# Optimization experiments

Hardware: AMD Instinct MI355X
Metric: run time of the kernel (lower is better)

Reference implementation:

```python
import jax, jax.numpy as jnp
import numpy as np

SEQ_LEN = 4096
EMBED_DIM = 1280
NUM_HEADS = 16
HEAD_DIM = EMBED_DIM // NUM_HEADS  # 80
SCALING = float(np.sqrt(HEAD_DIM))  # NOTE: source multiplies by sqrt(head_dim)
NEG_INF = float(np.finfo(np.float32).min)


def rotate_half(x):
    x1, x2 = jnp.split(x, 2, axis=-1)
    return jnp.concatenate((-x2, x1), axis=-1)


def setup_inputs() -> dict:
    key = jax.random.key(0)
    ks = jax.random.split(key, 7)
    s = 0.02
    hidden_states = jax.random.normal(ks[0], (SEQ_LEN, EMBED_DIM), dtype=jnp.float32)
    w_qkv = jax.random.normal(ks[1], (3 * EMBED_DIM, EMBED_DIM), dtype=jnp.float32) * s
    b_qkv = jax.random.normal(ks[2], (3 * EMBED_DIM,), dtype=jnp.float32) * s
    w_proj = jax.random.normal(ks[3], (EMBED_DIM, EMBED_DIM), dtype=jnp.float32) * s
    b_proj = jax.random.normal(ks[4], (EMBED_DIM,), dtype=jnp.float32) * s
    # rotary angles: theta duplicated to head_dim (emb = cat(rope, rope))
    inv_freq = 1.0 / (10000.0 ** (jnp.arange(0, HEAD_DIM // 2, dtype=jnp.float32) * 2.0 / HEAD_DIM))
    pos = jnp.arange(SEQ_LEN, dtype=jnp.float32)
    freqs = pos[:, None] * inv_freq[None, :]            # [S, hd/2]
    emb = jnp.concatenate((freqs, freqs), axis=-1)       # [S, hd]
    cos = jnp.cos(emb)
    sin = jnp.sin(emb)
    # 4 packed images of 1024 patches each
    cu_seqlens = jnp.array([0, 1024, 2048, 3072, 4096], dtype=jnp.int32)
    return {
        "hidden_states": hidden_states,
        "w_qkv": w_qkv, "b_qkv": b_qkv,
        "w_proj": w_proj, "b_proj": b_proj,
        "cos": cos, "sin": sin,
        "cu_seqlens": cu_seqlens,
    }


def reference(hidden_states, w_qkv, b_qkv, w_proj, b_proj, cos, sin, cu_seqlens):
    S = hidden_states.shape[0]
    # packed QKV projection
    qkv = hidden_states @ w_qkv.T + b_qkv                  # [S, 3D]
    qkv = qkv.reshape(S, 3, NUM_HEADS, HEAD_DIM)
    q, k, v = qkv[:, 0], qkv[:, 1], qkv[:, 2]              # [S, H, hd]
    # fp32 RoPE (broadcast cos/sin over heads)
    c = cos[:, None, :].astype(jnp.float32)
    sn = sin[:, None, :].astype(jnp.float32)
    qf, kf = q.astype(jnp.float32), k.astype(jnp.float32)
    q = (qf * c + rotate_half(qf) * sn).astype(q.dtype)
    k = (kf * c + rotate_half(kf) * sn).astype(k.dtype)
    # block-diagonal mask from cu_seqlens: same segment -> 0, else -inf
    pos = jnp.arange(S)
    seg = jnp.searchsorted(cu_seqlens, pos, side="right") - 1  # [S]
    bias = jnp.where(seg[:, None] == seg[None, :], 0.0, NEG_INF)  # [S, S]
    # dense attention over whole packed sequence (as in source)
    scores = jnp.einsum("shd,thd->hst", q, k) * SCALING + bias[None]
    weights = jax.nn.softmax(scores.astype(jnp.float32), axis=-1).astype(q.dtype)
    attn = jnp.einsum("hst,thd->shd", weights, v).reshape(S, EMBED_DIM)
    return attn @ w_proj.T + b_proj
```

## Files before the change

kernel.cpp:

```cpp
#include <hip/hip_runtime.h>

#define SEQ   4096
#define EMB   1280
#define NH    16
#define HD    80
#define HDP   96
#define O3    3840
#define SEGLEN 1024
#define NSEG  4
#define QSCALE (8.94427190999915878564f * 1.44269504088896340736f)

typedef unsigned short u16;
typedef __attribute__((ext_vector_type(8))) _Float16 f16x8;
typedef __attribute__((ext_vector_type(4))) _Float16 f16x4;
typedef __attribute__((ext_vector_type(2))) __fp16   h16x2;
typedef __attribute__((ext_vector_type(4))) float    f32x4;

__device__ __forceinline__ float ex2(float x) { return __builtin_amdgcn_exp2f(x); }

__device__ __forceinline__ u16 f2h(float f) {
  union { _Float16 h; u16 u; } v; v.h = (_Float16)f; return v.u;
}
__device__ __forceinline__ float h2f(u16 b) {
  union { u16 u; _Float16 h; } v; v.u = b; return (float)v.h;
}
__device__ __forceinline__ f32x4 exp2_4(f32x4 x) {
  f32x4 r; r.x = ex2(x.x); r.y = ex2(x.y); r.z = ex2(x.z); r.w = ex2(x.w); return r;
}
__device__ __forceinline__ f16x4 pk4(f32x4 s) {
  union { h16x2 h[2]; f16x4 f; } u;
  u.h[0] = __builtin_amdgcn_cvt_pkrtz(s.x, s.y);
  u.h[1] = __builtin_amdgcn_cvt_pkrtz(s.z, s.w);
  return u.f;
}
__device__ __forceinline__ void gl2lds16(const u16* g, u16* l) {
  __builtin_amdgcn_global_load_lds(
      (const __attribute__((address_space(1))) unsigned int*)g,
      (__attribute__((address_space(3))) unsigned int*)l, 16, 0, 0);
}

#define CVT_N1 (SEQ * EMB / 4)
#define CVT_N2 (O3 * EMB / 4)
#define CVT_N3 (EMB * EMB / 4)
__global__ void cvt_all_kernel(const float* __restrict__ a, const float* __restrict__ b,
                               const float* __restrict__ c, u16* __restrict__ oa,
                               u16* __restrict__ ob, u16* __restrict__ oc) {
  int i = blockIdx.x * blockDim.x + threadIdx.x;
  const float* src; u16* dst; int j = i;
  if (j < CVT_N1)                { src = a; dst = oa; }
  else if (j < CVT_N1 + CVT_N2)  { src = b; dst = ob; j -= CVT_N1; }
  else                           { src = c; dst = oc; j -= CVT_N1 + CVT_N2; }
  float4 f = ((const float4*)src)[j];
  union { u16 h[4]; uint2 v; } o;
  o.h[0] = f2h(f.x); o.h[1] = f2h(f.y); o.h[2] = f2h(f.z); o.h[3] = f2h(f.w);
  ((uint2*)dst)[j] = o.v;
}

template<int OUTF>
__global__ __launch_bounds__(256)
void gemm_bias_kernel(const u16* __restrict__ A, const u16* __restrict__ W,
                      const float* __restrict__ bias, void* __restrict__ Cout,
                      int N, int K) {
  __shared__ u16 As[128][64];
  __shared__ u16 Bs[128][64];
  const int tid  = threadIdx.x;
  const int bm   = blockIdx.y, bn = blockIdx.x;
  const int lane = tid & 63;
  const int wid  = tid >> 6;
  const int wm   = (wid >> 1) * 64, wn = (wid & 1) * 64;
  const int lr   = lane & 15, quad = lane >> 4;

  f32x4 acc[4][4];
  const f32x4 z4 = {0.f, 0.f, 0.f, 0.f};
  #pragma unroll
  for (int i = 0; i < 4; ++i)
    #pragma unroll
    for (int j = 0; j < 4; ++j) acc[i][j] = z4;

  const int arow = tid >> 3;
  const int acol = (((tid & 7) ^ (arow & 7)) * 8);
  const u16* Ab = A + (size_t)(bm * 128) * K;
  const u16* Wb = W + (size_t)(bn * 128) * K;
  u16* AsL = &As[0][0] + tid * 8;
  u16* BsL = &Bs[0][0] + tid * 8;

  for (int kt = 0; kt < K; kt += 64) {
    #pragma unroll
    for (int r = 0; r < 4; ++r) {
      gl2lds16(&Ab[(size_t)(arow + r * 32) * K + kt + acol], AsL + r * 2048);
      gl2lds16(&Wb[(size_t)(arow + r * 32) * K + kt + acol], BsL + r * 2048);
    }
    __syncthreads();
    #pragma unroll
    for (int k32 = 0; k32 < 2; ++k32) {
      const int c = (((k32 * 4 + quad) ^ (lr & 7)) * 8);
      f16x8 aF[4], bF[4];
      #pragma unroll
      for (int i = 0; i < 4; ++i) {
        aF[i] = *(const f16x8*)&As[wm + i * 16 + lr][c];
        bF[i] = *(const f16x8*)&Bs[wn + i * 16 + lr][c];
      }
      #pragma unroll
      for (int i = 0; i < 4; ++i)
        #pragma unroll
        for (int j = 0; j < 4; ++j)
          acc[i][j] = __builtin_amdgcn_mfma_f32_16x16x32_f16(aF[i], bF[j], acc[i][j], 0, 0, 0);
    }
    __syncthreads();
  }

  #pragma unroll
  for (int i = 0; i < 4; ++i) {
    int rowb = bm * 128 + wm + i * 16 + quad * 4;
    #pragma unroll
    for (int j = 0; j < 4; ++j) {
      int col = bn * 128 + wn + j * 16 + lr;
      float bv = bias[col];
      #pragma unroll
      for (int r = 0; r < 4; ++r) {
        float v = acc[i][j][r] + bv;
        if (OUTF) ((float*)Cout)[(size_t)(rowb + r) * N + col] = v;
        else      ((u16*)Cout)[(size_t)(rowb + r) * N + col] = f2h(v);
      }
    }
  }
}

__global__ __launch_bounds__(512, 2)
void gemm256_kernel(const u16* __restrict__ A, const u16* __restrict__ W,
                    const float* __restrict__ bias, u16* __restrict__ Cout,
                    int N, int K) {
  __shared__ u16 As[2][256][64];
  __shared__ u16 Bs[2][256][64];
  const int tid  = threadIdx.x;
  const int bm   = blockIdx.y, bn = blockIdx.x;
  const int lane = tid & 63;
  const int wid  = tid >> 6;
  const int wm   = wid >> 2;
  const int wn   = wid & 3;
  const int lr   = lane & 15, quad = lane >> 4;
  const int NT   = K >> 6;

  const u16* Ab = A + (size_t)(bm * 256) * K;
  const u16* Wb = W + (size_t)(bn * 256) * K;

  const int srr  = tid >> 3;
  const int scol = ((tid & 7) ^ (srr & 7)) << 3;
  const u16* ApL = Ab + (size_t)srr * K + scol;
  const u16* WpL = Wb + (size_t)srr * K + scol;

  auto stA = [&](int b, int row0, int t) {
    gl2lds16(ApL + (size_t)row0 * K + t * 64,        &As[b][row0][0]      + tid * 8);
    gl2lds16(ApL + (size_t)(row0 + 64) * K + t * 64, &As[b][row0 + 64][0] + tid * 8);
  };
  auto stB = [&](int b, int row0, int t) {
    gl2lds16(WpL + (size_t)row0 * K + t * 64,        &Bs[b][row0][0]      + tid * 8);
    gl2lds16(WpL + (size_t)(row0 + 64) * K + t * 64, &Bs[b][row0 + 64][0] + tid * 8);
  };

  f32x4 acc[8][4];
  const f32x4 z4 = {0.f, 0.f, 0.f, 0.f};
  #pragma unroll
  for (int i = 0; i < 8; ++i)
    #pragma unroll
    for (int j = 0; j < 4; ++j) acc[i][j] = z4;

  stA(0, 0, 0); stA(0, 128, 0);
  stB(0, 0, 0); stB(0, 128, 0);
  stA(1, 0, 1);
  asm volatile("s_waitcnt vmcnt(2)" ::: "memory");
  __builtin_amdgcn_s_barrier();

  for (int t = 0; t < NT; ++t) {
    const int buf = t & 1, nb = buf ^ 1;
    #pragma unroll
    for (int mq = 0; mq < 2; ++mq) {
      #pragma unroll
      for (int k32 = 0; k32 < 2; ++k32) {
        const int c = (((k32 * 4 + quad) ^ (lr & 7)) << 3);
        f16x8 aF[4], bF[4];
        #pragma unroll
        for (int i = 0; i < 4; ++i)
          aF[i] = *(const f16x8*)&As[buf][mq * 128 + wm * 64 + i * 16 + lr][c];
        #pragma unroll
        for (int j = 0; j < 4; ++j)
          bF[j] = *(const f16x8*)&Bs[buf][wn * 64 + j * 16 + lr][c];
        __builtin_amdgcn_sched_barrier(0);
        if (mq == 0 && k32 == 0) {
          if (t + 1 < NT) { stB(nb, 0, t + 1); stA(nb, 128, t + 1); }
        } else if (mq == 0 && k32 == 1) {
          if (t + 1 < NT) stB(nb, 128, t + 1);
        } else if (mq == 1 && k32 == 0) {
          if (t + 2 < NT) stA(buf, 0, t + 2);
        }
        __builtin_amdgcn_s_barrier();
        asm volatile("s_waitcnt lgkmcnt(0)" ::: "memory");
        __builtin_amdgcn_sched_barrier(0);
        __builtin_amdgcn_s_setprio(1);
        #pragma unroll
        for (int i = 0; i < 4; ++i)
          #pragma unroll
          for (int j = 0; j < 4; ++j)
            acc[mq * 4 + i][j] =
                __builtin_amdgcn_mfma_f32_16x16x32_f16(aF[i], bF[j], acc[mq * 4 + i][j], 0, 0, 0);
        __builtin_amdgcn_s_setprio(0);
        if (mq == 1 && k32 == 1) {
          if (t < NT - 2) asm volatile("s_waitcnt vmcnt(2)" ::: "memory");
          else            asm volatile("s_waitcnt vmcnt(0)" ::: "memory");
        }
        __builtin_amdgcn_s_barrier();
        __builtin_amdgcn_sched_barrier(0);
      }
    }
  }

  #pragma unroll
  for (int mq = 0; mq < 2; ++mq) {
    #pragma unroll
    for (int i = 0; i < 4; ++i) {
      const int rowb = bm * 256 + mq * 128 + wm * 64 + i * 16 + quad * 4;
      #pragma unroll
      for (int j = 0; j < 4; ++j) {
        const int col = bn * 256 + wn * 64 + j * 16 + lr;
        const float bv = bias[col];
        #pragma unroll
        for (int r = 0; r < 4; ++r)
          Cout[(size_t)(rowb + r) * N + col] = f2h(acc[mq * 4 + i][j][r] + bv);
      }
    }
  }
}

__global__ __launch_bounds__(256)
void rope_reorg_kernel(const u16* __restrict__ qkv, const float* __restrict__ cosp,
                       const float* __restrict__ sinp, u16* __restrict__ Qp,
                       u16* __restrict__ Kp, u16* __restrict__ Vt) {
  __shared__ u16 Qs[64][80];
  __shared__ u16 Ks[64][80];
  __shared__ u16 Vs[64][88];
  const int tid = threadIdx.x;
  const int s0 = blockIdx.x * 64;
  const int h  = blockIdx.y;

  for (int t = tid; t < 640; t += 256) {
    int r = t / 10, c = (t % 10) * 8;
    size_t g = (size_t)(s0 + r) * O3 + h * HD + c;
    *(uint4*)&Qs[r][c] = *(const uint4*)&qkv[g];
    *(uint4*)&Ks[r][c] = *(const uint4*)&qkv[g + EMB];
    *(uint4*)&Vs[r][c] = *(const uint4*)&qkv[g + 2 * EMB];
  }
  __syncthreads();

  for (int t = tid; t < 64 * 24; t += 256) {
    int r = t / 24, d4 = (t % 24) * 4;
    int s = s0 + r;
    size_t po = ((size_t)h * SEQ + s) * HDP + d4;
    if (d4 >= HD) {
      uint2 z = make_uint2(0, 0);
      *(uint2*)&Qp[po] = z; *(uint2*)&Kp[po] = z;
      continue;
    }
    float4 cv = *(const float4*)&cosp[(size_t)s * HD + d4];
    float4 sv = *(const float4*)&sinp[(size_t)s * HD + d4];
    int dp4 = (d4 < 40) ? d4 + 40 : d4 - 40;
    float sgn = (d4 < 40) ? -1.f : 1.f;
    union { u16 h[4]; uint2 v; } oq, ok;
    const float* cp = (const float*)&cv;
    const float* sp = (const float*)&sv;
    #pragma unroll
    for (int j = 0; j < 4; ++j) {
      float q  = h2f(Qs[r][d4 + j]),  k  = h2f(Ks[r][d4 + j]);
      float qp = h2f(Qs[r][dp4 + j]), kp = h2f(Ks[r][dp4 + j]);
      oq.h[j] = f2h((q * cp[j] + sgn * qp * sp[j]) * QSCALE);
      ok.h[j] = f2h(k * cp[j] + sgn * kp * sp[j]);
    }
    *(uint2*)&Qp[po] = oq.v;
    *(uint2*)&Kp[po] = ok.v;
  }

  for (int t = tid; t < HD * 8; t += 256) {
    int d = t / 8, sc = (t % 8) * 8;
    union { u16 h[8]; uint4 v; } o;
    #pragma unroll
    for (int j = 0; j < 8; ++j) o.h[j] = Vs[sc + j][d];
    *(uint4*)&Vt[((size_t)(h * HD + d)) * SEQ + s0 + sc] = o.v;
  }
}

__global__ __launch_bounds__(256)
void attn_kernel(const u16* __restrict__ Qp, const u16* __restrict__ Kp,
                 const u16* __restrict__ Vt, u16* __restrict__ attnO) {
  __shared__ u16 K_l[64][96];
  __shared__ u16 V_l[80][64];

  const int tid = threadIdx.x;
  const int lane = tid & 63, w = tid >> 6;
  const int lr = lane & 15, quad = lane >> 4;
  const int h = blockIdx.y, sg = blockIdx.z;
  const int seg0 = sg * SEGLEN;
  const int q0b = seg0 + blockIdx.x * 64;

  f16x8 qF[3];
  {
    int qrow = q0b + w * 16 + lr;
    #pragma unroll
    for (int kc = 0; kc < 3; ++kc)
      qF[kc] = *(const f16x8*)&Qp[((size_t)h * SEQ + qrow) * HDP + kc * 32 + quad * 8];
  }

  const u16* Kbase = Kp + ((size_t)h * SEQ + seg0) * HDP;
  const u16* Vbase = Vt + (size_t)h * HD * SEQ + seg0;
  const u16* pK[3]; u16* dK[3];
  const u16* pV[3]; u16* dV[3];
  #pragma unroll
  for (int t = 0; t < 3; ++t) {
    int s = t * 256 + tid;
    int r = s / 12, c = s % 12;
    pK[t] = Kbase + (size_t)r * HDP + c * 8;
    dK[t] = &K_l[0][0] + s * 8;
    int rv = s / 8, cv = s % 8;
    int cg = cv ^ (rv & 7);
    pV[t] = Vbase + (size_t)rv * SEQ + cg * 8;
    dV[t] = &V_l[0][0] + s * 8;
  }

  const f32x4 z4 = {0.f, 0.f, 0.f, 0.f};
  float m_r = -3.0e38f;
  float l_r = 0.0f;
  f32x4 Oacc[5];
  #pragma unroll
  for (int n = 0; n < 5; ++n) Oacc[n] = z4;

  for (int kt = 0; kt < SEGLEN; kt += 64) {
    gl2lds16(pK[0], dK[0]); gl2lds16(pK[1], dK[1]); gl2lds16(pK[2], dK[2]);
    gl2lds16(pV[0], dV[0]); gl2lds16(pV[1], dV[1]);
    if (tid < 128) gl2lds16(pV[2], dV[2]);
    #pragma unroll
    for (int t = 0; t < 3; ++t) { pK[t] += 64 * HDP; pV[t] += 64; }
    __syncthreads();

    f32x4 S[4];
    #pragma unroll
    for (int ct = 0; ct < 4; ++ct) {
      S[ct] = z4;
      #pragma unroll
      for (int kc = 0; kc < 3; ++kc) {
        f16x8 kF = *(const f16x8*)&K_l[ct * 16 + lr][kc * 32 + quad * 8];
        S[ct] = __builtin_amdgcn_mfma_f32_16x16x32_f16(kF, qF[kc], S[ct], 0, 0, 0);
      }
    }

    float mx = fmaxf(fmaxf(S[0].x, S[0].y), fmaxf(S[0].z, S[0].w));
    #pragma unroll
    for (int ct = 1; ct < 4; ++ct)
      mx = fmaxf(mx, fmaxf(fmaxf(S[ct].x, S[ct].y), fmaxf(S[ct].z, S[ct].w)));
    mx = fmaxf(mx, __shfl_xor(mx, 16, 64));
    mx = fmaxf(mx, __shfl_xor(mx, 32, 64));
    float mnew = fmaxf(m_r, mx);
    float alpha = ex2(m_r - mnew);
    m_r = mnew;

    f32x4 mv = {mnew, mnew, mnew, mnew};
    float rs = 0.f;
    #pragma unroll
    for (int ct = 0; ct < 4; ++ct) {
      S[ct] = exp2_4(S[ct] - mv);
      rs += (S[ct].x + S[ct].y) + (S[ct].z + S[ct].w);
    }
    rs += __shfl_xor(rs, 16, 64);
    rs += __shfl_xor(rs, 32, 64);
    l_r = l_r * alpha + rs;

    if (__ballot(alpha != 1.0f)) {
      f32x4 al;
      al.x = __shfl(alpha, quad * 4 + 0, 64);
      al.y = __shfl(alpha, quad * 4 + 1, 64);
      al.z = __shfl(alpha, quad * 4 + 2, 64);
      al.w = __shfl(alpha, quad * 4 + 3, 64);
      #pragma unroll
      for (int n = 0; n < 5; ++n) Oacc[n] *= al;
    }

    f16x4 pF[4];
    #pragma unroll
    for (int ct = 0; ct < 4; ++ct) pF[ct] = pk4(S[ct]);

    #pragma unroll
    for (int ct = 0; ct < 4; ++ct) {
      const int cchunk = 2 * ct + (quad >> 1);
      #pragma unroll
      for (int n = 0; n < 5; ++n) {
        int vrow = n * 16 + lr;
        const u16* vp = &V_l[0][0] + vrow * 64 + ((cchunk ^ (vrow & 7)) << 3) + ((quad & 1) << 2);
        f16x4 vF = *(const f16x4*)vp;
        Oacc[n] = __builtin_amdgcn_mfma_f32_16x16x16f16(pF[ct], vF, Oacc[n], 0, 0, 0);
      }
    }
    __syncthreads();
  }

  f32x4 linv;
  linv.x = 1.0f / __shfl(l_r, quad * 4 + 0, 64);
  linv.y = 1.0f / __shfl(l_r, quad * 4 + 1, 64);
  linv.z = 1.0f / __shfl(l_r, quad * 4 + 2, 64);
  linv.w = 1.0f / __shfl(l_r, quad * 4 + 3, 64);
  #pragma unroll
  for (int n = 0; n < 5; ++n) {
    int rowb = q0b + w * 16 + quad * 4;
    int col = h * HD + n * 16 + lr;
    attnO[(size_t)(rowb + 0) * EMB + col] = f2h(Oacc[n].x * linv.x);
    attnO[(size_t)(rowb + 1) * EMB + col] = f2h(Oacc[n].y * linv.y);
    attnO[(size_t)(rowb + 2) * EMB + col] = f2h(Oacc[n].z * linv.z);
    attnO[(size_t)(rowb + 3) * EMB + col] = f2h(Oacc[n].w * linv.w);
  }
}

extern "C" void kernel_launch(void* const* d_in, const int* in_sizes, int n_in,
                              void* d_out, int out_size, void* d_ws, size_t ws_size,
                              hipStream_t stream) {
  const float* hs     = (const float*)d_in[0];
  const float* w_qkv  = (const float*)d_in[1];
  const float* b_qkv  = (const float*)d_in[2];
  const float* w_proj = (const float*)d_in[3];
  const float* b_proj = (const float*)d_in[4];
  const float* cosp   = (const float*)d_in[5];
  const float* sinp   = (const float*)d_in[6];
  float* out = (float*)d_out;

  char* p = (char*)d_ws;
  auto take = [&](size_t bytes) { char* q = p; p += (bytes + 255) & ~(size_t)255; return q; };
  u16* hsH    = (u16*)take((size_t)SEQ * EMB * 2);
  u16* wqkvH  = (u16*)take((size_t)O3 * EMB * 2);
  u16* wprojH = (u16*)take((size_t)EMB * EMB * 2);
  u16* qkvO   = (u16*)take((size_t)SEQ * O3 * 2);
  u16* Qp     = (u16*)take((size_t)NH * SEQ * HDP * 2);
  u16* Kp     = (u16*)take((size_t)NH * SEQ * HDP * 2);
  u16* Vt     = (u16*)take((size_t)NH * HD * SEQ * 2);
  u16* attnH  = (u16*)take((size_t)SEQ * EMB * 2);

  int ncvt = (CVT_N1 + CVT_N2 + CVT_N3) / 256;
  cvt_all_kernel<<<ncvt, 256, 0, stream>>>(hs, w_qkv, w_proj, hsH, wqkvH, wprojH);

  gemm256_kernel<<<dim3(O3 / 256, SEQ / 256), 512, 0, stream>>>(hsH, wqkvH, b_qkv, qkvO, O3, EMB);

  rope_reorg_kernel<<<dim3(SEQ / 64, NH), 256, 0, stream>>>(qkvO, cosp, sinp, Qp, Kp, Vt);

  attn_kernel<<<dim3(SEGLEN / 64, NH, NSEG), 256, 0, stream>>>(Qp, Kp, Vt, attnH);

  gemm_bias_kernel<1><<<dim3(EMB / 128, SEQ / 128), 256, 0, stream>>>(attnH, wprojH, b_proj, out, EMB, EMB);
}
```

Measured before the change: 244.2 us.

## Double-buffer K/V LDS tiles, swizzle K layout, and raise MFMA priority

```diff
diff --git a/kernel.cpp b/kernel.cpp
--- a/kernel.cpp
+++ b/kernel.cpp
@@ -290,8 +290,10 @@
 __global__ __launch_bounds__(256)
 void attn_kernel(const u16* __restrict__ Qp, const u16* __restrict__ Kp,
                  const u16* __restrict__ Vt, u16* __restrict__ attnO) {
-  __shared__ u16 K_l[64][96];
-  __shared__ u16 V_l[80][64];
+  __shared__ u16 K_l[2][64][96];
+  __shared__ u16 V_l[2][80][64];
+  const int KSZ = 64 * 96;
+  const int VSZ = 80 * 64;
 
   const int tid = threadIdx.x;
   const int lane = tid & 63, w = tid >> 6;
@@ -316,13 +318,25 @@
   for (int t = 0; t < 3; ++t) {
     int s = t * 256 + tid;
     int r = s / 12, c = s % 12;
-    pK[t] = Kbase + (size_t)r * HDP + c * 8;
-    dK[t] = &K_l[0][0] + s * 8;
+    int ck = (c & ~3) | ((c & 3) ^ ((r >> 1) & 3));
+    pK[t] = Kbase + (size_t)r * HDP + ck * 8;
+    dK[t] = &K_l[0][0][0] + s * 8;
     int rv = s / 8, cv = s % 8;
     int cg = cv ^ (rv & 7);
     pV[t] = Vbase + (size_t)rv * SEQ + cg * 8;
-    dV[t] = &V_l[0][0] + s * 8;
-  }
+    dV[t] = &V_l[0][0][0] + s * 8;
+  }
+
+  auto stage_adv = [&](int b) {
+    gl2lds16(pK[0], dK[0] + b * KSZ);
+    gl2lds16(pK[1], dK[1] + b * KSZ);
+    gl2lds16(pK[2], dK[2] + b * KSZ);
+    gl2lds16(pV[0], dV[0] + b * VSZ);
+    gl2lds16(pV[1], dV[1] + b * VSZ);
+    if (tid < 128) gl2lds16(pV[2], dV[2] + b * VSZ);
+    #pragma unroll
+    for (int t = 0; t < 3; ++t) { pK[t] += 64 * HDP; pV[t] += 64; }
+  };
 
   const f32x4 z4 = {0.f, 0.f, 0.f, 0.f};
   float m_r = -3.0e38f;
@@ -331,24 +345,29 @@
   #pragma unroll
   for (int n = 0; n < 5; ++n) Oacc[n] = z4;
 
+  const int kswz = (lr >> 1) & 3;
+
+  stage_adv(0);
+  asm volatile("s_waitcnt vmcnt(0)" ::: "memory");
+  __builtin_amdgcn_s_barrier();
+  __builtin_amdgcn_sched_barrier(0);
+
   for (int kt = 0; kt < SEGLEN; kt += 64) {
-    gl2lds16(pK[0], dK[0]); gl2lds16(pK[1], dK[1]); gl2lds16(pK[2], dK[2]);
-    gl2lds16(pV[0], dV[0]); gl2lds16(pV[1], dV[1]);
-    if (tid < 128) gl2lds16(pV[2], dV[2]);
-    #pragma unroll
-    for (int t = 0; t < 3; ++t) { pK[t] += 64 * HDP; pV[t] += 64; }
-    __syncthreads();
+    const int buf = (kt >> 6) & 1;
+    if (kt + 64 < SEGLEN) stage_adv(buf ^ 1);
 
     f32x4 S[4];
+    __builtin_amdgcn_s_setprio(1);
     #pragma unroll
     for (int ct = 0; ct < 4; ++ct) {
       S[ct] = z4;
       #pragma unroll
       for (int kc = 0; kc < 3; ++kc) {
-        f16x8 kF = *(const f16x8*)&K_l[ct * 16 + lr][kc * 32 + quad * 8];
+        f16x8 kF = *(const f16x8*)&K_l[buf][ct * 16 + lr][kc * 32 + ((quad ^ kswz) << 3)];
         S[ct] = __builtin_amdgcn_mfma_f32_16x16x32_f16(kF, qF[kc], S[ct], 0, 0, 0);
       }
     }
+    __builtin_amdgcn_s_setprio(0);
 
     float mx = fmaxf(fmaxf(S[0].x, S[0].y), fmaxf(S[0].z, S[0].w));
     #pragma unroll
@@ -385,18 +404,23 @@
     #pragma unroll
     for (int ct = 0; ct < 4; ++ct) pF[ct] = pk4(S[ct]);
 
+    __builtin_amdgcn_s_setprio(1);
     #pragma unroll
     for (int ct = 0; ct < 4; ++ct) {
       const int cchunk = 2 * ct + (quad >> 1);
       #pragma unroll
       for (int n = 0; n < 5; ++n) {
         int vrow = n * 16 + lr;
-        const u16* vp = &V_l[0][0] + vrow * 64 + ((cchunk ^ (vrow & 7)) << 3) + ((quad & 1) << 2);
+        const u16* vp = &V_l[buf][0][0] + vrow * 64 + ((cchunk ^ (vrow & 7)) << 3) + ((quad & 1) << 2);
         f16x4 vF = *(const f16x4*)vp;
         Oacc[n] = __builtin_amdgcn_mfma_f32_16x16x16f16(pF[ct], vF, Oacc[n], 0, 0, 0);
       }
     }
-    __syncthreads();
+    __builtin_amdgcn_s_setprio(0);
+
+    asm volatile("s_waitcnt vmcnt(0)" ::: "memory");
+    __builtin_amdgcn_s_barrier();
+    __builtin_amdgcn_sched_barrier(0);
   }
 
   f32x4 linv;
```

After: 253.0 us. 1.04x slower.

## Compute softmax row sums via MFMA with ones column; swizzle K LDS; setprio

Applied to the files above, without the earlier changes.

```diff
diff --git a/kernel.cpp b/kernel.cpp
--- a/kernel.cpp
+++ b/kernel.cpp
@@ -291,7 +291,7 @@
 void attn_kernel(const u16* __restrict__ Qp, const u16* __restrict__ Kp,
                  const u16* __restrict__ Vt, u16* __restrict__ attnO) {
   __shared__ u16 K_l[64][96];
-  __shared__ u16 V_l[80][64];
+  __shared__ u16 V_l[96][64];
 
   const int tid = threadIdx.x;
   const int lane = tid & 63, w = tid >> 6;
@@ -308,6 +308,12 @@
       qF[kc] = *(const f16x8*)&Qp[((size_t)h * SEQ + qrow) * HDP + kc * 32 + quad * 8];
   }
 
+  {
+    u16 val = (tid < 16) ? (u16)0x3C00 : (u16)0;
+    u16* q = &V_l[80][0] + tid * 4;
+    q[0] = val; q[1] = val; q[2] = val; q[3] = val;
+  }
+
   const u16* Kbase = Kp + ((size_t)h * SEQ + seg0) * HDP;
   const u16* Vbase = Vt + (size_t)h * HD * SEQ + seg0;
   const u16* pK[3]; u16* dK[3];
@@ -316,7 +322,8 @@
   for (int t = 0; t < 3; ++t) {
     int s = t * 256 + tid;
     int r = s / 12, c = s % 12;
-    pK[t] = Kbase + (size_t)r * HDP + c * 8;
+    int ck = (c & ~3) | ((c & 3) ^ ((r >> 1) & 3));
+    pK[t] = Kbase + (size_t)r * HDP + ck * 8;
     dK[t] = &K_l[0][0] + s * 8;
     int rv = s / 8, cv = s % 8;
     int cg = cv ^ (rv & 7);
@@ -326,10 +333,11 @@
 
   const f32x4 z4 = {0.f, 0.f, 0.f, 0.f};
   float m_r = -3.0e38f;
-  float l_r = 0.0f;
-  f32x4 Oacc[5];
-  #pragma unroll
-  for (int n = 0; n < 5; ++n) Oacc[n] = z4;
+  f32x4 Oacc[6];
+  #pragma unroll
+  for (int n = 0; n < 6; ++n) Oacc[n] = z4;
+
+  const int kswz = (lr >> 1) & 3;
 
   for (int kt = 0; kt < SEGLEN; kt += 64) {
     gl2lds16(pK[0], dK[0]); gl2lds16(pK[1], dK[1]); gl2lds16(pK[2], dK[2]);
@@ -340,15 +348,17 @@
     __syncthreads();
 
     f32x4 S[4];
+    __builtin_amdgcn_s_setprio(1);
     #pragma unroll
     for (int ct = 0; ct < 4; ++ct) {
       S[ct] = z4;
       #pragma unroll
       for (int kc = 0; kc < 3; ++kc) {
-        f16x8 kF = *(const f16x8*)&K_l[ct * 16 + lr][kc * 32 + quad * 8];
+        f16x8 kF = *(const f16x8*)&K_l[ct * 16 + lr][kc * 32 + ((quad ^ kswz) << 3)];
         S[ct] = __builtin_amdgcn_mfma_f32_16x16x32_f16(kF, qF[kc], S[ct], 0, 0, 0);
       }
     }
+    __builtin_amdgcn_s_setprio(0);
 
     float mx = fmaxf(fmaxf(S[0].x, S[0].y), fmaxf(S[0].z, S[0].w));
     #pragma unroll
@@ -361,15 +371,8 @@
     m_r = mnew;
 
     f32x4 mv = {mnew, mnew, mnew, mnew};
-    float rs = 0.f;
-    #pragma unroll
-    for (int ct = 0; ct < 4; ++ct) {
-      S[ct] = exp2_4(S[ct] - mv);
-      rs += (S[ct].x + S[ct].y) + (S[ct].z + S[ct].w);
-    }
-    rs += __shfl_xor(rs, 16, 64);
-    rs += __shfl_xor(rs, 32, 64);
-    l_r = l_r * alpha + rs;
+    #pragma unroll
+    for (int ct = 0; ct < 4; ++ct) S[ct] = exp2_4(S[ct] - mv);
 
     if (__ballot(alpha != 1.0f)) {
       f32x4 al;
@@ -378,32 +381,34 @@
       al.z = __shfl(alpha, quad * 4 + 2, 64);
       al.w = __shfl(alpha, quad * 4 + 3, 64);
       #pragma unroll
-      for (int n = 0; n < 5; ++n) Oacc[n] *= al;
+      for (int n = 0; n < 6; ++n) Oacc[n] *= al;
     }
 
     f16x4 pF[4];
     #pragma unroll
     for (int ct = 0; ct < 4; ++ct) pF[ct] = pk4(S[ct]);
 
+    __builtin_amdgcn_s_setprio(1);
     #pragma unroll
     for (int ct = 0; ct < 4; ++ct) {
       const int cchunk = 2 * ct + (quad >> 1);
       #pragma unroll
-      for (int n = 0; n < 5; ++n) {
+      for (int n = 0; n < 6; ++n) {
         int vrow = n * 16 + lr;
         const u16* vp = &V_l[0][0] + vrow * 64 + ((cchunk ^ (vrow & 7)) << 3) + ((quad & 1) << 2);
         f16x4 vF = *(const f16x4*)vp;
         Oacc[n] = __builtin_amdgcn_mfma_f32_16x16x16f16(pF[ct], vF, Oacc[n], 0, 0, 0);
       }
     }
+    __builtin_amdgcn_s_setprio(0);
     __syncthreads();
   }
 
   f32x4 linv;
-  linv.x = 1.0f / __shfl(l_r, quad * 4 + 0, 64);
-  linv.y = 1.0f / __shfl(l_r, quad * 4 + 1, 64);
-  linv.z = 1.0f / __shfl(l_r, quad * 4 + 2, 64);
-  linv.w = 1.0f / __shfl(l_r, quad * 4 + 3, 64);
+  linv.x = 1.0f / __shfl(Oacc[5].x, quad << 4, 64);
+  linv.y = 1.0f / __shfl(Oacc[5].y, quad << 4, 64);
+  linv.z = 1.0f / __shfl(Oacc[5].z, quad << 4, 64);
+  linv.w = 1.0f / __shfl(Oacc[5].w, quad << 4, 64);
   #pragma unroll
   for (int n = 0; n < 5; ++n) {
     int rowb = q0b + w * 16 + quad * 4;
```

Measured after the change: 238.4 us. -2.4%, faster.
